# Kernel optimization log

Hardware: AMD Instinct MI355X
Metric: run time of the kernel (lower is better)

The kernel has to match this reference:

```python
import jax, jax.numpy as jnp
import numpy as np

D_MODEL = 2048
NUM_HEADS = 32
NUM_KV_HEADS = 8
DIM_HEAD = D_MODEL // NUM_HEADS  # 64
REPS = NUM_HEADS // NUM_KV_HEADS  # 4
B, T = 2, 2048


def setup_inputs() -> dict:
    key = jax.random.key(0)
    k_x, k_q, k_k, k_v, k_o = jax.random.split(key, 5)
    s = 1.0 / np.sqrt(D_MODEL)
    return {
        "x": jax.random.normal(k_x, (B, T, D_MODEL), dtype=jnp.float32),
        "wq": jax.random.normal(k_q, (D_MODEL, NUM_HEADS * DIM_HEAD), dtype=jnp.float32) * s,
        "wk": jax.random.normal(k_k, (D_MODEL, NUM_KV_HEADS * DIM_HEAD), dtype=jnp.float32) * s,
        "wv": jax.random.normal(k_v, (D_MODEL, NUM_KV_HEADS * DIM_HEAD), dtype=jnp.float32) * s,
        "wo": jax.random.normal(k_o, (D_MODEL, D_MODEL), dtype=jnp.float32) * s,
    }


def reference(x, wq, wk, wv, wo):
    Bb, Tt, _ = x.shape
    q = (x @ wq).reshape(Bb, Tt, NUM_HEADS, DIM_HEAD)       # [B,T,H,dh]
    k = (x @ wk).reshape(Bb, Tt, NUM_KV_HEADS, DIM_HEAD)    # [B,T,Hkv,dh]
    v = (x @ wv).reshape(Bb, Tt, NUM_KV_HEADS, DIM_HEAD)
    # repeat_interleave KV heads to match Q heads
    k = jnp.repeat(k, REPS, axis=2)                          # [B,T,H,dh]
    v = jnp.repeat(v, REPS, axis=2)
    scale = 1.0 / np.sqrt(DIM_HEAD).astype(np.float32)
    scores = jnp.einsum('bqhd,bkhd->bhqk', q, k) * scale     # [B,H,T,T]
    causal = jnp.tril(jnp.ones((Tt, Tt), dtype=bool))
    scores = jnp.where(causal, scores, -jnp.inf)
    attn = jax.nn.softmax(scores, axis=-1)
    out = jnp.einsum('bhqk,bkhd->bqhd', attn, v)             # [B,T,H,dh]
    out = out.reshape(Bb, Tt, NUM_HEADS * DIM_HEAD)
    return out @ wo
```

## Files before the change

### kernel.cpp

```cpp
#include <hip/hip_runtime.h>

typedef unsigned short u16;
typedef unsigned int u32;
typedef unsigned long long u64;

typedef __bf16 bf16x8 __attribute__((ext_vector_type(8)));
typedef float f32x4 __attribute__((ext_vector_type(4)));
typedef u16 u16x4 __attribute__((ext_vector_type(4)));

__device__ __forceinline__ u16 f2bf(float f) {
  u32 u = __builtin_bit_cast(u32, f);
  u += 0x7fffu + ((u >> 16) & 1u);
  return (u16)(u >> 16);
}

__device__ __forceinline__ u32 packbf2(float a, float b) {
  __bf16 x = (__bf16)a, y = (__bf16)b;
  return (u32)__builtin_bit_cast(u16, x) | ((u32)__builtin_bit_cast(u16, y) << 16);
}

__device__ __forceinline__ float fexp2(float x) {
#if __has_builtin(__builtin_amdgcn_exp2f)
  return __builtin_amdgcn_exp2f(x);
#else
  return exp2f(x);
#endif
}

__device__ __forceinline__ void gload_lds16(const void* g, void* lds) {
  __builtin_amdgcn_global_load_lds(
      (const __attribute__((address_space(1))) void*)g,
      (__attribute__((address_space(3))) void*)lds, 16, 0, 0);
}

#define QSCALE 0.18033688011112043f

__global__ __launch_bounds__(256) void prep_kernel(
    const float* __restrict__ x, u16* __restrict__ xb,
    const float* __restrict__ wq, const float* __restrict__ wk,
    const float* __restrict__ wv, const float* __restrict__ wo,
    u16* __restrict__ wqT, u16* __restrict__ wkT,
    u16* __restrict__ wvT, u16* __restrict__ woT) {
  __shared__ float tile[32][33];
  int bid = blockIdx.x;
  if (bid < 8192) {
    int i = (bid * 256 + threadIdx.x) * 4;
    float4 v = *reinterpret_cast<const float4*>(x + i);
    u16x4 o;
    o[0] = f2bf(v.x); o[1] = f2bf(v.y); o[2] = f2bf(v.z); o[3] = f2bf(v.w);
    *reinterpret_cast<u16x4*>(xb + i) = o;
    return;
  }
  bid -= 8192;
  constexpr int K = 2048;
  const float* w_;
  u16* wt;
  int N;
  switch (bid >> 12) {
    case 0: w_ = wq; wt = wqT; N = 2048; break;
    case 1: w_ = wo; wt = woT; N = 2048; break;
    case 2: w_ = wk; wt = wkT; N = 512; break;
    default: w_ = wv; wt = wvT; N = 512; break;
  }
  int rem = bid & 4095;
  int bx = (rem & 63) * 32;
  if (bx >= N) return;
  int by = (rem >> 6) * 32;
  int tx = threadIdx.x & 31, ty = threadIdx.x >> 5;
#pragma unroll
  for (int i = 0; i < 32; i += 8)
    tile[ty + i][tx] = w_[(size_t)(by + ty + i) * N + bx + tx];
  __syncthreads();
#pragma unroll
  for (int i = 0; i < 32; i += 8)
    wt[(size_t)(bx + ty + i) * K + by + tx] = f2bf(tile[tx][ty + i]);
}

template <int MODE>
__global__ __launch_bounds__(512, 2) void gemm256(
    const u16* __restrict__ A, const u16* __restrict__ BT,
    float* __restrict__ Cf, u16* __restrict__ Cb, u16* __restrict__ Cb2,
    u16* __restrict__ Cb3, int M, int N) {
  constexpr int K = 2048, NT = 32;
  __shared__ __align__(16) u16 Ab[2][256 * 64];
  __shared__ __align__(16) u16 Bb[2][256 * 64];
  const int t = threadIdx.x;
  const int lane = t & 63;
  const int w = t >> 6;
  const int wm = w >> 2, wn = w & 3;
  const int l15 = lane & 15, l4 = lane >> 4;

  const int nwg = gridDim.x * gridDim.y;
  const int bid = blockIdx.y * gridDim.x + blockIdx.x;
  const int wg = (bid & 7) * (nwg >> 3) + (bid >> 3);
  const int brow = (wg / gridDim.x) * 256;
  const int bcol = (wg % gridDim.x) * 256;

  const int r0 = t >> 3;
  const int gc = ((t & 7) ^ (r0 & 7)) * 8;
  auto stageA = [&](int q, int h, int kt) {
    const u16* src = A + (size_t)(brow + h * 128 + r0) * K + kt * 64 + gc;
    u16* dst = &Ab[q][(h * 128 + r0) * 64 + (t & 7) * 8];
    gload_lds16(src, dst);
    gload_lds16(src + (size_t)64 * K, dst + 64 * 64);
  };
  auto stageB = [&](int q, int h, int kt) {
    const u16* src = BT + (size_t)(bcol + h * 128 + r0) * K + kt * 64 + gc;
    u16* dst = &Bb[q][(h * 128 + r0) * 64 + (t & 7) * 8];
    gload_lds16(src, dst);
    gload_lds16(src + (size_t)64 * K, dst + 64 * 64);
  };

  f32x4 acc[8][4];
#pragma unroll
  for (int mi = 0; mi < 8; mi++)
#pragma unroll
    for (int n = 0; n < 4; n++)
#pragma unroll
      for (int r = 0; r < 4; r++) acc[mi][n][r] = 0.f;

  stageA(0, 0, 0); stageA(0, 1, 0);
  stageB(0, 0, 0); stageB(0, 1, 0);
  stageA(1, 0, 1); stageA(1, 1, 1);
  asm volatile("s_waitcnt vmcnt(4)" ::: "memory");
  __builtin_amdgcn_sched_barrier(0);
  __builtin_amdgcn_s_barrier();

  for (int kt = 0; kt < NT; ++kt) {
    const int q = kt & 1;
    const u16* Al = Ab[q];
    const u16* Bl = Bb[q];
    bf16x8 af[8][2], bf[4][2];

#pragma unroll
    for (int m = 0; m < 4; ++m) {
      int row = wm * 128 + m * 16 + l15;
#pragma unroll
      for (int ks = 0; ks < 2; ++ks)
        af[m][ks] = *reinterpret_cast<const bf16x8*>(
            &Al[row * 64 + (((ks * 4 + l4) ^ (row & 7)) * 8)]);
    }
#pragma unroll
    for (int n = 0; n < 2; ++n) {
      int row = wn * 64 + n * 16 + l15;
#pragma unroll
      for (int ks = 0; ks < 2; ++ks)
        bf[n][ks] = *reinterpret_cast<const bf16x8*>(
            &Bl[row * 64 + (((ks * 4 + l4) ^ (row & 7)) * 8)]);
    }
    if (kt + 1 < NT) stageB(q ^ 1, 0, kt + 1);
    __builtin_amdgcn_s_barrier();
    __builtin_amdgcn_s_setprio(1);
#pragma unroll
    for (int ks = 0; ks < 2; ++ks)
#pragma unroll
      for (int m = 0; m < 4; ++m)
#pragma unroll
        for (int n = 0; n < 2; ++n)
          acc[m][n] = __builtin_amdgcn_mfma_f32_16x16x32_bf16(
              af[m][ks], bf[n][ks], acc[m][n], 0, 0, 0);
    __builtin_amdgcn_s_setprio(0);
    __builtin_amdgcn_s_barrier();

#pragma unroll
    for (int m = 4; m < 8; ++m) {
      int row = wm * 128 + m * 16 + l15;
#pragma unroll
      for (int ks = 0; ks < 2; ++ks)
        af[m][ks] = *reinterpret_cast<const bf16x8*>(
            &Al[row * 64 + (((ks * 4 + l4) ^ (row & 7)) * 8)]);
    }
#pragma unroll
    for (int n = 2; n < 4; ++n) {
      int row = wn * 64 + n * 16 + l15;
#pragma unroll
      for (int ks = 0; ks < 2; ++ks)
        bf[n][ks] = *reinterpret_cast<const bf16x8*>(
            &Bl[row * 64 + (((ks * 4 + l4) ^ (row & 7)) * 8)]);
    }
    if (kt + 1 < NT) stageB(q ^ 1, 1, kt + 1);
    __builtin_amdgcn_s_barrier();
    __builtin_amdgcn_s_setprio(1);
#pragma unroll
    for (int ks = 0; ks < 2; ++ks)
#pragma unroll
      for (int m = 0; m < 4; ++m)
#pragma unroll
        for (int n = 2; n < 4; ++n)
          acc[m][n] = __builtin_amdgcn_mfma_f32_16x16x32_bf16(
              af[m][ks], bf[n][ks], acc[m][n], 0, 0, 0);
    __builtin_amdgcn_s_setprio(0);
    __builtin_amdgcn_s_barrier();

    if (kt + 2 < NT) stageA(q, 0, kt + 2);
    __builtin_amdgcn_s_barrier();
    __builtin_amdgcn_s_setprio(1);
#pragma unroll
    for (int ks = 0; ks < 2; ++ks)
#pragma unroll
      for (int m = 4; m < 8; ++m)
#pragma unroll
        for (int n = 0; n < 2; ++n)
          acc[m][n] = __builtin_amdgcn_mfma_f32_16x16x32_bf16(
              af[m][ks], bf[n][ks], acc[m][n], 0, 0, 0);
    __builtin_amdgcn_s_setprio(0);
    __builtin_amdgcn_s_barrier();

    if (kt + 2 < NT) stageA(q, 1, kt + 2);
    __builtin_amdgcn_s_barrier();
    __builtin_amdgcn_s_setprio(1);
#pragma unroll
    for (int ks = 0; ks < 2; ++ks)
#pragma unroll
      for (int m = 4; m < 8; ++m)
#pragma unroll
        for (int n = 2; n < 4; ++n)
          acc[m][n] = __builtin_amdgcn_mfma_f32_16x16x32_bf16(
              af[m][ks], bf[n][ks], acc[m][n], 0, 0, 0);
    __builtin_amdgcn_s_setprio(0);
    if (kt + 2 < NT) {
      asm volatile("s_waitcnt vmcnt(4)" ::: "memory");
    } else {
      asm volatile("s_waitcnt vmcnt(0)" ::: "memory");
    }
    __builtin_amdgcn_sched_barrier(0);
    __builtin_amdgcn_s_barrier();
  }

#pragma unroll
  for (int mi = 0; mi < 8; ++mi) {
    int grow0 = brow + wm * 128 + mi * 16 + l4 * 4;
#pragma unroll
    for (int n = 0; n < 4; ++n) {
      int gcol = bcol + wn * 64 + n * 16 + l15;
      if (MODE == 1) {
#pragma unroll
        for (int r = 0; r < 4; ++r)
          Cf[(size_t)(grow0 + r) * N + gcol] = acc[mi][n][r];
      } else if (bcol < 2048) {
#pragma unroll
        for (int r = 0; r < 4; ++r)
          Cb[(size_t)(grow0 + r) * 2048 + gcol] = f2bf(acc[mi][n][r] * QSCALE);
      } else if (bcol < 2560) {
#pragma unroll
        for (int r = 0; r < 4; ++r)
          Cb2[(size_t)(grow0 + r) * 512 + (gcol - 2048)] = f2bf(acc[mi][n][r]);
      } else {
        int col = gcol - 2560;
        int bb = grow0 >> 11, tt = grow0 & 2047;
        u64 wv = (u64)packbf2(acc[mi][n][0], acc[mi][n][1]) |
                 ((u64)packbf2(acc[mi][n][2], acc[mi][n][3]) << 32);
        *reinterpret_cast<u64*>(&Cb3[((size_t)(bb * 512 + col)) * 2048 + tt]) = wv;
      }
    }
  }
}

__global__ __launch_bounds__(512, 2) void gemm256n(
    const u16* __restrict__ A, const u16* __restrict__ BT,
    float* __restrict__ Cf, int M, int N) {
  constexpr int K = 2048, NT = 32;
  __shared__ __align__(16) u16 Ab[2][256 * 64];
  __shared__ __align__(16) u16 Bb[2][128 * 64];
  const int t = threadIdx.x;
  const int lane = t & 63;
  const int w = t >> 6;
  const int wm = w >> 1, wn = w & 1;
  const int l15 = lane & 15, l4 = lane >> 4;

  const int nwg = gridDim.x * gridDim.y;
  const int bid = blockIdx.y * gridDim.x + blockIdx.x;
  const int wg = (bid & 7) * (nwg >> 3) + (bid >> 3);
  const int brow = (wg / gridDim.x) * 256;
  const int bcol = (wg % gridDim.x) * 128;

  const int r0 = t >> 3;
  const int gc = ((t & 7) ^ (r0 & 7)) * 8;
  auto stageA = [&](int q, int h, int kt) {
    const u16* src = A + (size_t)(brow + h * 128 + r0) * K + kt * 64 + gc;
    u16* dst = &Ab[q][(h * 128 + r0) * 64 + (t & 7) * 8];
    gload_lds16(src, dst);
    gload_lds16(src + (size_t)64 * K, dst + 64 * 64);
  };
  auto stageB = [&](int q, int h, int kt) {
    const u16* src = BT + (size_t)(bcol + h * 64 + r0) * K + kt * 64 + gc;
    u16* dst = &Bb[q][(h * 64 + r0) * 64 + (t & 7) * 8];
    gload_lds16(src, dst);
  };

  f32x4 acc[4][4];
#pragma unroll
  for (int m = 0; m < 4; m++)
#pragma unroll
    for (int n = 0; n < 4; n++)
#pragma unroll
      for (int r = 0; r < 4; r++) acc[m][n][r] = 0.f;

  stageA(0, 0, 0); stageA(0, 1, 0);
  stageB(0, 0, 0); stageB(0, 1, 0);
  stageA(1, 0, 1); stageA(1, 1, 1);
  asm volatile("s_waitcnt vmcnt(4)" ::: "memory");
  __builtin_amdgcn_sched_barrier(0);
  __builtin_amdgcn_s_barrier();

  for (int kt = 0; kt < NT; ++kt) {
    const int q = kt & 1;
    const u16* Al = Ab[q];
    const u16* Bl = Bb[q];
    bf16x8 af[4][2], bf[4][2];

#pragma unroll
    for (int m = 0; m < 2; ++m) {
      int row = wm * 64 + m * 16 + l15;
#pragma unroll
      for (int ks = 0; ks < 2; ++ks)
        af[m][ks] = *reinterpret_cast<const bf16x8*>(
            &Al[row * 64 + (((ks * 4 + l4) ^ (row & 7)) * 8)]);
    }
#pragma unroll
    for (int n = 0; n < 2; ++n) {
      int row = wn * 64 + n * 16 + l15;
#pragma unroll
      for (int ks = 0; ks < 2; ++ks)
        bf[n][ks] = *reinterpret_cast<const bf16x8*>(
            &Bl[row * 64 + (((ks * 4 + l4) ^ (row & 7)) * 8)]);
    }
    if (kt + 1 < NT) stageB(q ^ 1, 0, kt + 1);
    __builtin_amdgcn_s_barrier();
    __builtin_amdgcn_s_setprio(1);
#pragma unroll
    for (int ks = 0; ks < 2; ++ks)
#pragma unroll
      for (int m = 0; m < 2; ++m)
#pragma unroll
        for (int n = 0; n < 2; ++n)
          acc[m][n] = __builtin_amdgcn_mfma_f32_16x16x32_bf16(
              af[m][ks], bf[n][ks], acc[m][n], 0, 0, 0);
    __builtin_amdgcn_s_setprio(0);
    __builtin_amdgcn_s_barrier();

#pragma unroll
    for (int m = 2; m < 4; ++m) {
      int row = wm * 64 + m * 16 + l15;
#pragma unroll
      for (int ks = 0; ks < 2; ++ks)
        af[m][ks] = *reinterpret_cast<const bf16x8*>(
            &Al[row * 64 + (((ks * 4 + l4) ^ (row & 7)) * 8)]);
    }
#pragma unroll
    for (int n = 2; n < 4; ++n) {
      int row = wn * 64 + n * 16 + l15;
#pragma unroll
      for (int ks = 0; ks < 2; ++ks)
        bf[n][ks] = *reinterpret_cast<const bf16x8*>(
            &Bl[row * 64 + (((ks * 4 + l4) ^ (row & 7)) * 8)]);
    }
    if (kt + 1 < NT) stageB(q ^ 1, 1, kt + 1);
    __builtin_amdgcn_s_barrier();
    __builtin_amdgcn_s_setprio(1);
#pragma unroll
    for (int ks = 0; ks < 2; ++ks)
#pragma unroll
      for (int m = 0; m < 2; ++m)
#pragma unroll
        for (int n = 2; n < 4; ++n)
          acc[m][n] = __builtin_amdgcn_mfma_f32_16x16x32_bf16(
              af[m][ks], bf[n][ks], acc[m][n], 0, 0, 0);
    __builtin_amdgcn_s_setprio(0);
    __builtin_amdgcn_s_barrier();

    if (kt + 2 < NT) stageA(q, 0, kt + 2);
    __builtin_amdgcn_s_barrier();
    __builtin_amdgcn_s_setprio(1);
#pragma unroll
    for (int ks = 0; ks < 2; ++ks)
#pragma unroll
      for (int m = 2; m < 4; ++m)
#pragma unroll
        for (int n = 0; n < 2; ++n)
          acc[m][n] = __builtin_amdgcn_mfma_f32_16x16x32_bf16(
              af[m][ks], bf[n][ks], acc[m][n], 0, 0, 0);
    __builtin_amdgcn_s_setprio(0);
    __builtin_amdgcn_s_barrier();

    if (kt + 2 < NT) stageA(q, 1, kt + 2);
    __builtin_amdgcn_s_barrier();
    __builtin_amdgcn_s_setprio(1);
#pragma unroll
    for (int ks = 0; ks < 2; ++ks)
#pragma unroll
      for (int m = 2; m < 4; ++m)
#pragma unroll
        for (int n = 2; n < 4; ++n)
          acc[m][n] = __builtin_amdgcn_mfma_f32_16x16x32_bf16(
              af[m][ks], bf[n][ks], acc[m][n], 0, 0, 0);
    __builtin_amdgcn_s_setprio(0);
    if (kt + 2 < NT) {
      asm volatile("s_waitcnt vmcnt(4)" ::: "memory");
    } else {
      asm volatile("s_waitcnt vmcnt(0)" ::: "memory");
    }
    __builtin_amdgcn_sched_barrier(0);
    __builtin_amdgcn_s_barrier();
  }

#pragma unroll
  for (int m = 0; m < 4; ++m) {
    int grow0 = brow + wm * 64 + m * 16 + l4 * 4;
#pragma unroll
    for (int n = 0; n < 4; ++n) {
      int gcol = bcol + wn * 64 + n * 16 + l15;
#pragma unroll
      for (int r = 0; r < 4; ++r)
        Cf[(size_t)(grow0 + r) * N + gcol] = acc[m][n][r];
    }
  }
}

__global__ __launch_bounds__(256, 4) void attn_kernel(
    const u16* __restrict__ Qb, const u16* __restrict__ Kb,
    const u16* __restrict__ VT, u16* __restrict__ Ob) {
  const int bx = blockIdx.x;
  const int kvh = bx & 7;
  const int u = bx >> 3;
  const int jj = u & 15;
  const int v = u >> 4;
  const int h = kvh * 4 + (v & 3);
  const int b = v >> 2;
  const int t = threadIdx.x;
  const int lane = t & 63;
  const int w = t >> 6;
  const int q15 = lane & 15, g = lane >> 4;

  __shared__ __align__(16) u16 Ks[2][64 * 64];
  __shared__ __align__(16) u16 Vs[2][64 * 64];
  __shared__ __align__(16) u32 Pu[4][16 * 32];

  const size_t Krow0 = (size_t)b * 2048;
  const size_t Vrow0 = ((size_t)b * 8 + kvh) * 64;

  u16* const dk0 = &Ks[0][t * 8];
  u16* const dk1 = &Ks[1][t * 8];
  u16* const dv0 = &Vs[0][t * 8];
  u16* const dv1 = &Vs[1][t * 8];
  const int row0 = t >> 3;
  const int gcs = ((t & 7) ^ (row0 & 7)) * 8;
  const u16* const pk0 = Kb + (Krow0 + row0) * 512 + kvh * 64 + gcs;
  const u16* const pv0 = VT + (Vrow0 + row0) * 2048 + gcs;
  const u16* kp = pk0;
  const u16* vp = pv0;

  auto stage = [&](int buf, const u16* kpp, const u16* vpp) {
    u16* dk = buf ? dk1 : dk0;
    u16* dv = buf ? dv1 : dv0;
    gload_lds16(kpp, dk);
    gload_lds16(kpp + 32 * 512, dk + 2048);
    gload_lds16(vpp, dv);
    gload_lds16(vpp + 32 * 2048, dv + 2048);
  };

  const int swzB = (q15 & 7) << 3;
  const int swzP = (q15 & 7) << 2;
  u32* const pw = &Pu[w][0];
  const int nA = 32 - jj;
  const int nsteps = 33;

  stage(0, kp, vp);
  __syncthreads();
  int cur = 0;
  int ss = 0;

#pragma unroll
  for (int ph = 0; ph < 2; ++ph) {
    const int qt = ph ? jj : 31 - jj;
    const int nkv = qt + 1;
    const int wq0 = qt * 64 + w * 16;

    bf16x8 qf[2];
    {
      const u16* q0 = &Qb[((size_t)b * 2048 + wq0 + q15) * 2048 + h * 64 + g * 8];
      qf[0] = *reinterpret_cast<const bf16x8*>(q0);
      qf[1] = *reinterpret_cast<const bf16x8*>(q0 + 32);
    }

    f32x4 oo[4];
#pragma unroll
    for (int c = 0; c < 4; c++)
#pragma unroll
      for (int r = 0; r < 4; r++) oo[c][r] = 0.f;
    float mr = -1e30f, lr = 0.f;

    for (int kv = 0; kv < nkv; ++kv, ++ss) {
      const int kvbase = kv << 6;
      if (ss + 1 < nsteps) {
        if (ss + 1 == nA) {
          kp = pk0;
          vp = pv0;
        } else {
          kp += 64 * 512;
          vp += 64;
        }
        stage(cur ^ 1, kp, vp);
      }

      f32x4 s[4];
#pragma unroll
      for (int c = 0; c < 4; c++)
#pragma unroll
        for (int r = 0; r < 4; r++) s[c][r] = 0.f;
      __builtin_amdgcn_s_setprio(1);
#pragma unroll
      for (int ks = 0; ks < 2; ++ks) {
        const int kcol = (ks * 32 + g * 8) ^ swzB;
#pragma unroll
        for (int c = 0; c < 4; c++) {
          bf16x8 kb = *reinterpret_cast<const bf16x8*>(
              &Ks[cur][(c * 16 + q15) * 64 + kcol]);
          s[c] = __builtin_amdgcn_mfma_f32_16x16x32_bf16(kb, qf[ks], s[c], 0, 0, 0);
        }
      }
      __builtin_amdgcn_s_setprio(0);

      if (kv == qt) {
        const int qg = wq0 + q15;
#pragma unroll
        for (int c = 0; c < 4; c++)
#pragma unroll
          for (int r = 0; r < 4; r++)
            if (kvbase + c * 16 + g * 4 + r > qg) s[c][r] = -1e30f;
      }

      float mx0 = fmaxf(fmaxf(s[0][0], s[0][1]), fmaxf(s[0][2], s[0][3]));
      float mx1 = fmaxf(fmaxf(s[1][0], s[1][1]), fmaxf(s[1][2], s[1][3]));
      float mx2 = fmaxf(fmaxf(s[2][0], s[2][1]), fmaxf(s[2][2], s[2][3]));
      float mx3 = fmaxf(fmaxf(s[3][0], s[3][1]), fmaxf(s[3][2], s[3][3]));
      float mx = fmaxf(fmaxf(mx0, mx1), fmaxf(mx2, mx3));
      mx = fmaxf(mx, __shfl_xor(mx, 16));
      mx = fmaxf(mx, __shfl_xor(mx, 32));
      if (!__all(mx <= mr + 8.f)) {
        float mnew = fmaxf(mr, mx);
        float alpha = fexp2(mr - mnew);
        lr *= alpha;
#pragma unroll
        for (int c = 0; c < 4; c++)
#pragma unroll
          for (int r = 0; r < 4; r++) oo[c][r] *= alpha;
        mr = mnew;
      }
      float p[4][4];
      float rs = 0.f;
#pragma unroll
      for (int c = 0; c < 4; c++) {
        float t0 = fexp2(s[c][0] - mr);
        float t1 = fexp2(s[c][1] - mr);
        float t2 = fexp2(s[c][2] - mr);
        float t3 = fexp2(s[c][3] - mr);
        p[c][0] = t0; p[c][1] = t1; p[c][2] = t2; p[c][3] = t3;
        rs += (t0 + t1) + (t2 + t3);
      }
      rs += __shfl_xor(rs, 16);
      rs += __shfl_xor(rs, 32);
      lr += rs;
#pragma unroll
      for (int c = 0; c < 4; c++) {
        u64 wv = (u64)packbf2(p[c][0], p[c][1]) |
                 ((u64)packbf2(p[c][2], p[c][3]) << 32);
        *reinterpret_cast<u64*>(&pw[q15 * 32 + ((c * 8 + g * 2) ^ swzP)]) = wv;
      }
      bf16x8 pb[2];
#pragma unroll
      for (int ks = 0; ks < 2; ++ks)
        pb[ks] = *reinterpret_cast<const bf16x8*>(
            &pw[q15 * 32 + ((ks * 16 + g * 4) ^ swzP)]);

      __builtin_amdgcn_s_setprio(1);
#pragma unroll
      for (int ks = 0; ks < 2; ++ks) {
        const int vcol = (ks * 32 + g * 8) ^ swzB;
#pragma unroll
        for (int c2 = 0; c2 < 4; c2++) {
          bf16x8 vb = *reinterpret_cast<const bf16x8*>(
              &Vs[cur][(c2 * 16 + q15) * 64 + vcol]);
          oo[c2] = __builtin_amdgcn_mfma_f32_16x16x32_bf16(vb, pb[ks], oo[c2], 0, 0, 0);
        }
      }
      __builtin_amdgcn_s_setprio(0);

      __syncthreads();
      cur ^= 1;
    }

    const int qq = lane >> 2, cl = lane & 3;
    const int swq = (qq & 7) << 2;
    {
      float rcp = 1.0f / lr;
#pragma unroll
      for (int c2 = 0; c2 < 4; c2++) {
        u64 wv = (u64)packbf2(oo[c2][0] * rcp, oo[c2][1] * rcp) |
                 ((u64)packbf2(oo[c2][2] * rcp, oo[c2][3] * rcp) << 32);
        *reinterpret_cast<u64*>(&pw[q15 * 32 + ((c2 * 8 + g * 2) ^ swzP)]) = wv;
      }
      uint4 d0 = *reinterpret_cast<const uint4*>(&pw[qq * 32 + ((cl * 4) ^ swq)]);
      uint4 d1 = *reinterpret_cast<const uint4*>(&pw[qq * 32 + ((cl * 4 + 16) ^ swq)]);
      u32* og = (u32*)Ob + ((size_t)b * 2048 + wq0 + qq) * 1024 + h * 32;
      *reinterpret_cast<uint4*>(&og[cl * 4]) = d0;
      *reinterpret_cast<uint4*>(&og[cl * 4 + 16]) = d1;
    }
  }
}

extern "C" void kernel_launch(void* const* d_in, const int* in_sizes, int n_in,
                              void* d_out, int out_size, void* d_ws, size_t ws_size,
                              hipStream_t stream) {
  const float* x = (const float*)d_in[0];
  const float* wq = (const float*)d_in[1];
  const float* wk = (const float*)d_in[2];
  const float* wv = (const float*)d_in[3];
  const float* wo = (const float*)d_in[4];
  float* out = (float*)d_out;

  char* p = (char*)d_ws;
  u16* xb = (u16*)p;   p += (size_t)4096 * 2048 * 2;
  u16* wqT = (u16*)p;  p += (size_t)2048 * 2048 * 2;
  u16* wkT = (u16*)p;  p += (size_t)512 * 2048 * 2;
  u16* wvT = (u16*)p;  p += (size_t)512 * 2048 * 2;
  u16* woT = (u16*)p;  p += (size_t)2048 * 2048 * 2;
  u16* Qb = (u16*)p;   p += (size_t)4096 * 2048 * 2;
  u16* Kb = (u16*)p;   p += (size_t)4096 * 512 * 2;
  u16* VTb = (u16*)p;  p += (size_t)2 * 512 * 2048 * 2;
  u16* attn = xb;

  prep_kernel<<<8192 + 16384, 256, 0, stream>>>(
      x, xb, wq, wk, wv, wo, wqT, wkT, wvT, woT);

  gemm256<3><<<dim3(3072 / 256, 4096 / 256), 512, 0, stream>>>(
      xb, wqT, nullptr, Qb, Kb, VTb, 4096, 3072);

  attn_kernel<<<1024, 256, 0, stream>>>(Qb, Kb, VTb, attn);

  gemm256n<<<dim3(2048 / 128, 4096 / 256), 512, 0, stream>>>(
      attn, woT, out, 4096, 2048);
}
```

Measured before the change: 191.2 us.

## Software-pipeline QK^T of next tile with softmax and PV of previous tile

Restructures the flash-attention inner loop so the QK^T MFMAs for tile kv are issued before the softmax and PV of tile kv-1. The V fragments are held in registers (vpr) across the barrier, and scores are carried in sp. The goal is to overlap exp/ALU softmax work with matrix-core work and hide LDS latency. The cost is higher register pressure (16 more bf16x8 V registers plus scores), which may lower occupancy. An extra __syncthreads is added after the output write.

After: 196.9 us. +3.0%, slower.

```diff
diff --git a/kernel.cpp b/kernel.cpp
--- a/kernel.cpp
+++ b/kernel.cpp
@@ -490,8 +490,70 @@
       for (int r = 0; r < 4; r++) oo[c][r] = 0.f;
     float mr = -1e30f, lr = 0.f;
 
+    f32x4 sp[4];
+    bf16x8 vpr[2][4];
+
+    auto softmax_pv = [&](bool domask, int kvbase) {
+      if (domask) {
+        const int qg = wq0 + q15;
+#pragma unroll
+        for (int c = 0; c < 4; c++)
+#pragma unroll
+          for (int r = 0; r < 4; r++)
+            if (kvbase + c * 16 + g * 4 + r > qg) sp[c][r] = -1e30f;
+      }
+      float mx0 = fmaxf(fmaxf(sp[0][0], sp[0][1]), fmaxf(sp[0][2], sp[0][3]));
+      float mx1 = fmaxf(fmaxf(sp[1][0], sp[1][1]), fmaxf(sp[1][2], sp[1][3]));
+      float mx2 = fmaxf(fmaxf(sp[2][0], sp[2][1]), fmaxf(sp[2][2], sp[2][3]));
+      float mx3 = fmaxf(fmaxf(sp[3][0], sp[3][1]), fmaxf(sp[3][2], sp[3][3]));
+      float mx = fmaxf(fmaxf(mx0, mx1), fmaxf(mx2, mx3));
+      mx = fmaxf(mx, __shfl_xor(mx, 16));
+      mx = fmaxf(mx, __shfl_xor(mx, 32));
+      if (!__all(mx <= mr + 8.f)) {
+        float mnew = fmaxf(mr, mx);
+        float alpha = fexp2(mr - mnew);
+        lr *= alpha;
+#pragma unroll
+        for (int c = 0; c < 4; c++)
+#pragma unroll
+          for (int r = 0; r < 4; r++) oo[c][r] *= alpha;
+        mr = mnew;
+      }
+      float p[4][4];
+      float rs = 0.f;
+#pragma unroll
+      for (int c = 0; c < 4; c++) {
+        float t0 = fexp2(sp[c][0] - mr);
+        float t1 = fexp2(sp[c][1] - mr);
+        float t2 = fexp2(sp[c][2] - mr);
+        float t3 = fexp2(sp[c][3] - mr);
+        p[c][0] = t0; p[c][1] = t1; p[c][2] = t2; p[c][3] = t3;
+        rs += (t0 + t1) + (t2 + t3);
+      }
+      rs += __shfl_xor(rs, 16);
+      rs += __shfl_xor(rs, 32);
+      lr += rs;
+#pragma unroll
+      for (int c = 0; c < 4; c++) {
+        u64 wv = (u64)packbf2(p[c][0], p[c][1]) |
+                 ((u64)packbf2(p[c][2], p[c][3]) << 32);
+        *reinterpret_cast<u64*>(&pw[q15 * 32 + ((c * 8 + g * 2) ^ swzP)]) = wv;
+      }
+      bf16x8 pb[2];
+#pragma unroll
+      for (int ks = 0; ks < 2; ++ks)
+        pb[ks] = *reinterpret_cast<const bf16x8*>(
+            &pw[q15 * 32 + ((ks * 16 + g * 4) ^ swzP)]);
+      __builtin_amdgcn_s_setprio(1);
+#pragma unroll
+      for (int ks = 0; ks < 2; ++ks)
+#pragma unroll
+        for (int c2 = 0; c2 < 4; c2++)
+          oo[c2] = __builtin_amdgcn_mfma_f32_16x16x32_bf16(vpr[ks][c2], pb[ks], oo[c2], 0, 0, 0);
+      __builtin_amdgcn_s_setprio(0);
+    };
+
     for (int kv = 0; kv < nkv; ++kv, ++ss) {
-      const int kvbase = kv << 6;
       if (ss + 1 < nsteps) {
         if (ss + 1 == nA) {
           kp = pk0;
@@ -503,11 +565,11 @@
         stage(cur ^ 1, kp, vp);
       }
 
-      f32x4 s[4];
+      f32x4 sn[4];
 #pragma unroll
       for (int c = 0; c < 4; c++)
 #pragma unroll
-        for (int r = 0; r < 4; r++) s[c][r] = 0.f;
+        for (int r = 0; r < 4; r++) sn[c][r] = 0.f;
       __builtin_amdgcn_s_setprio(1);
 #pragma unroll
       for (int ks = 0; ks < 2; ++ks) {
@@ -516,79 +578,29 @@
         for (int c = 0; c < 4; c++) {
           bf16x8 kb = *reinterpret_cast<const bf16x8*>(
               &Ks[cur][(c * 16 + q15) * 64 + kcol]);
-          s[c] = __builtin_amdgcn_mfma_f32_16x16x32_bf16(kb, qf[ks], s[c], 0, 0, 0);
+          sn[c] = __builtin_amdgcn_mfma_f32_16x16x32_bf16(kb, qf[ks], sn[c], 0, 0, 0);
         }
       }
       __builtin_amdgcn_s_setprio(0);
 
-      if (kv == qt) {
-        const int qg = wq0 + q15;
-#pragma unroll
-        for (int c = 0; c < 4; c++)
-#pragma unroll
-          for (int r = 0; r < 4; r++)
-            if (kvbase + c * 16 + g * 4 + r > qg) s[c][r] = -1e30f;
-      }
-
-      float mx0 = fmaxf(fmaxf(s[0][0], s[0][1]), fmaxf(s[0][2], s[0][3]));
-      float mx1 = fmaxf(fmaxf(s[1][0], s[1][1]), fmaxf(s[1][2], s[1][3]));
-      float mx2 = fmaxf(fmaxf(s[2][0], s[2][1]), fmaxf(s[2][2], s[2][3]));
-      float mx3 = fmaxf(fmaxf(s[3][0], s[3][1]), fmaxf(s[3][2], s[3][3]));
-      float mx = fmaxf(fmaxf(mx0, mx1), fmaxf(mx2, mx3));
-      mx = fmaxf(mx, __shfl_xor(mx, 16));
-      mx = fmaxf(mx, __shfl_xor(mx, 32));
-      if (!__all(mx <= mr + 8.f)) {
-        float mnew = fmaxf(mr, mx);
-        float alpha = fexp2(mr - mnew);
-        lr *= alpha;
-#pragma unroll
-        for (int c = 0; c < 4; c++)
-#pragma unroll
-          for (int r = 0; r < 4; r++) oo[c][r] *= alpha;
-        mr = mnew;
-      }
-      float p[4][4];
-      float rs = 0.f;
-#pragma unroll
-      for (int c = 0; c < 4; c++) {
-        float t0 = fexp2(s[c][0] - mr);
-        float t1 = fexp2(s[c][1] - mr);
-        float t2 = fexp2(s[c][2] - mr);
-        float t3 = fexp2(s[c][3] - mr);
-        p[c][0] = t0; p[c][1] = t1; p[c][2] = t2; p[c][3] = t3;
-        rs += (t0 + t1) + (t2 + t3);
-      }
-      rs += __shfl_xor(rs, 16);
-      rs += __shfl_xor(rs, 32);
-      lr += rs;
-#pragma unroll
-      for (int c = 0; c < 4; c++) {
-        u64 wv = (u64)packbf2(p[c][0], p[c][1]) |
-                 ((u64)packbf2(p[c][2], p[c][3]) << 32);
-        *reinterpret_cast<u64*>(&pw[q15 * 32 + ((c * 8 + g * 2) ^ swzP)]) = wv;
-      }
-      bf16x8 pb[2];
-#pragma unroll
-      for (int ks = 0; ks < 2; ++ks)
-        pb[ks] = *reinterpret_cast<const bf16x8*>(
-            &pw[q15 * 32 + ((ks * 16 + g * 4) ^ swzP)]);
-
-      __builtin_amdgcn_s_setprio(1);
+      if (kv > 0) softmax_pv(false, 0);
+
+#pragma unroll
+      for (int c = 0; c < 4; c++) sp[c] = sn[c];
 #pragma unroll
       for (int ks = 0; ks < 2; ++ks) {
         const int vcol = (ks * 32 + g * 8) ^ swzB;
 #pragma unroll
-        for (int c2 = 0; c2 < 4; c2++) {
-          bf16x8 vb = *reinterpret_cast<const bf16x8*>(
+        for (int c2 = 0; c2 < 4; c2++)
+          vpr[ks][c2] = *reinterpret_cast<const bf16x8*>(
               &Vs[cur][(c2 * 16 + q15) * 64 + vcol]);
-          oo[c2] = __builtin_amdgcn_mfma_f32_16x16x32_bf16(vb, pb[ks], oo[c2], 0, 0, 0);
-        }
-      }
-      __builtin_amdgcn_s_setprio(0);
+      }
 
       __syncthreads();
       cur ^= 1;
     }
+
+    softmax_pv(true, qt << 6);
 
     const int qq = lane >> 2, cl = lane & 3;
     const int swq = (qq & 7) << 2;
@@ -606,6 +618,7 @@
       *reinterpret_cast<uint4*>(&og[cl * 4]) = d0;
       *reinterpret_cast<uint4*>(&og[cl * 4 + 16]) = d1;
     }
+    __syncthreads();
   }
 }
 
```
